# Performance work log

Measured on AMD Instinct MI355X. Metric: run time of the kernel, lower is better.

The kernel has to match this reference:

```python
import jax, jax.numpy as jnp
import numpy as np

SP = 4      # sp_size (number of simulated sequence-parallel ranks)
NH = 16     # num_attention_heads
HD = 64     # head_dim
HS = 1024   # hidden_size
B = 1       # batch
S = 8192    # global sequence length (SP chunks of 2048)


def setup_inputs() -> dict:
    key = jax.random.key(0)
    ks = jax.random.split(key, 9)
    w_scale = 1.0 / np.sqrt(HS)
    def w(k):
        # xavier-ish init, stored as [in, out] so y = x @ W + b
        return jax.random.uniform(k, (HS, HS), jnp.float32, -w_scale, w_scale)
    return {
        'hidden_states': jax.random.normal(ks[0], (B, S, HS), jnp.float32),
        'Wq': w(ks[1]), 'bq': jnp.zeros((HS,), jnp.float32),
        'Wk': w(ks[2]), 'bk': jnp.zeros((HS,), jnp.float32),
        'Wv': w(ks[3]), 'bv': jnp.zeros((HS,), jnp.float32),
        'Wo': w(ks[4]), 'bo': jnp.zeros((HS,), jnp.float32),
    }


def reference(hidden_states, Wq, bq, Wk, bk, Wv, bv, Wo, bo):
    b, s, _ = hidden_states.shape
    sc = s // SP  # per-rank chunk length
    inv_sqrt_hd = 1.0 / np.sqrt(HD)

    def heads(x):
        # [B, S, HS] -> [SP, B, NH, Sc, HD]
        return x.reshape(b, SP, sc, NH, HD).transpose(1, 0, 3, 2, 4)

    q = heads(hidden_states @ Wq + bq)
    k = heads(hidden_states @ Wk + bk)
    v = heads(hidden_states @ Wv + bv)

    out = jnp.zeros_like(q)
    # ring attention: at step i each rank r attends to chunk (r + i) mod SP
    for i in range(SP):
        ki = jnp.roll(k, -i, axis=0)
        vi = jnp.roll(v, -i, axis=0)
        scores = jnp.einsum('sbhqd,sbhkd->sbhqk', q, ki) * inv_sqrt_hd
        probs = jax.nn.softmax(scores, axis=-1)  # per-chunk softmax (faithful to source)
        out = out + jnp.einsum('sbhqk,sbhkd->sbhqd', probs, vi)
    out = out / SP  # source divides accumulated context by sp_size

    # [SP, B, NH, Sc, HD] -> [B, S, NH*HD]
    ctx = out.transpose(1, 0, 3, 2, 4).reshape(b, s, NH * HD)
    return ctx @ Wo + bo
```

## Files before the change

### kernel.cpp

```cpp
#include <hip/hip_runtime.h>

#define DEVINL __device__ __forceinline__

typedef __attribute__((ext_vector_type(8))) short short8;
typedef __attribute__((ext_vector_type(4))) float floatx4;
typedef __attribute__((ext_vector_type(2))) unsigned uintx2;
typedef __attribute__((ext_vector_type(8))) _Float16 halfx8;

DEVINL unsigned short f2bf(float f){
  unsigned u = __builtin_bit_cast(unsigned, f);
  u += 0x7FFFu + ((u >> 16) & 1u);
  return (unsigned short)(u >> 16);
}
DEVINL unsigned pk2(float a, float b){
  unsigned ua = __builtin_bit_cast(unsigned, a);
  unsigned ub = __builtin_bit_cast(unsigned, b);
  ua += 0x7FFFu + ((ua >> 16) & 1u);
  ub += 0x7FFFu + ((ub >> 16) & 1u);
  return (ua >> 16) | (ub & 0xFFFF0000u);
}
DEVINL unsigned pkfast(float a, float b){
  unsigned ua = __builtin_bit_cast(unsigned, a) + 0x8000u;
  unsigned ub = __builtin_bit_cast(unsigned, b) + 0x8000u;
  return __builtin_amdgcn_perm(ub, ua, 0x07060302u);
}
DEVINL unsigned pkh(float a, float b){
  return __builtin_bit_cast(unsigned, __builtin_amdgcn_cvt_pkrtz(a, b));
}
DEVINL float bf2f(unsigned short h){
  unsigned u = ((unsigned)h) << 16;
  return __builtin_bit_cast(float, u);
}
DEVINL void gload_lds16(const void* g, void* l){
  __builtin_amdgcn_global_load_lds((const __attribute__((address_space(1))) void*)g,
                                   (__attribute__((address_space(3))) void*)l, 16, 0, 0);
}
DEVINL int perm2(int k){
  return (((k >> 4) & 1) << 5) | (((k >> 2) & 3) << 3) | (((k >> 5) & 1) << 2) | (k & 3);
}

__global__ void k_detect(const unsigned* __restrict__ w, int* __restrict__ flag){
  __shared__ int cnt;
  if (threadIdx.x == 0) cnt = 0;
  __syncthreads();
  int c = 0;
  for (int i = threadIdx.x; i < 1024; i += 256){
    unsigned e = (w[i] >> 7) & 0xFFu;
    c += (e >= 120u && e <= 132u) ? 1 : 0;
  }
  atomicAdd(&cnt, c);
  __syncthreads();
  if (threadIdx.x == 0) *flag = (cnt > 512) ? 1 : 0;
}

__global__ void k_conv_bf16(const void* __restrict__ src, unsigned short* __restrict__ dst,
                            int n, const int* __restrict__ flag){
  int i = (blockIdx.x * 256 + threadIdx.x) * 8;
  if (i >= n) return;
  if (*flag){
    ((uint4*)dst)[i >> 3] = ((const uint4*)src)[i >> 3];
  } else {
    const float* s = (const float*)src;
    short8 v;
    #pragma unroll
    for (int j = 0; j < 8; j++) v[j] = (short)f2bf(s[i + j]);
    *(short8*)(dst + i) = v;
  }
}

__global__ void k_conv_wT4(const void* __restrict__ s0, const void* __restrict__ s1,
                           const void* __restrict__ s2, const void* __restrict__ s3,
                           unsigned short* __restrict__ d0, unsigned short* __restrict__ d1,
                           unsigned short* __restrict__ d2, unsigned short* __restrict__ d3,
                           const int* __restrict__ flag){
  __shared__ float tile[32][33];
  const void* src; unsigned short* dst;
  switch (blockIdx.z){
    case 0: src = s0; dst = d0; break;
    case 1: src = s1; dst = d1; break;
    case 2: src = s2; dst = d2; break;
    default: src = s3; dst = d3; break;
  }
  const int tx = threadIdx.x & 31, ty = threadIdx.x >> 5;
  const int bx = blockIdx.x, by = blockIdx.y;
  const int isbf = *flag;
  #pragma unroll
  for (int r = 0; r < 32; r += 8){
    int k = by*32 + ty + r, n = bx*32 + tx;
    float v = isbf ? bf2f(((const unsigned short*)src)[k*1024 + n])
                   : ((const float*)src)[k*1024 + n];
    tile[ty + r][tx] = v;
  }
  __syncthreads();
  #pragma unroll
  for (int r = 0; r < 32; r += 8){
    int n = bx*32 + ty + r, k = by*32 + tx;
    dst[n*1024 + k] = f2bf(tile[tx][ty + r]);
  }
}

__global__ void k_conv_b4(const void* __restrict__ s0, const void* __restrict__ s1,
                          const void* __restrict__ s2, const void* __restrict__ s3,
                          float* __restrict__ dst, const int* __restrict__ flag){
  int i = blockIdx.x * 256 + threadIdx.x;
  if (i >= 4096) return;
  int z = i >> 10, j = i & 1023;
  const void* s = (z == 0) ? s0 : (z == 1) ? s1 : (z == 2) ? s2 : s3;
  dst[i] = (*flag) ? bf2f(((const unsigned short*)s)[j]) : ((const float*)s)[j];
}

template<int MODE>
__global__ __launch_bounds__(256, 2) void k_gemm(
    const unsigned short* __restrict__ A, const unsigned short* __restrict__ Bt,
    const float* __restrict__ bias, void* __restrict__ C0, void* __restrict__ C1,
    void* __restrict__ C2, const int* __restrict__ flagp, float scale)
{
  const int K = 1024;
  __shared__ __align__(16) unsigned short As[128*32];
  __shared__ __align__(16) unsigned short Bs[128*32];
  const int tid = threadIdx.x;
  const int lane = tid & 63, wave = tid >> 6;
  const int quad = lane >> 4, l15 = lane & 15;
  const int m0 = blockIdx.x * 128, n0 = blockIdx.y * 128;
  const int wm = (wave >> 1) * 64, wn = (wave & 1) * 64;
  const floatx4 fzero = {0.f, 0.f, 0.f, 0.f};
  floatx4 acc[4][4];
  #pragma unroll
  for (int i = 0; i < 4; i++)
    #pragma unroll
    for (int j = 0; j < 4; j++) acc[i][j] = fzero;

  for (int k0 = 0; k0 < K; k0 += 32){
    __syncthreads();
    #pragma unroll
    for (int rep = 0; rep < 2; rep++){
      int idx = tid + rep*256;
      int row = idx >> 2, c = idx & 3;
      gload_lds16(A  + (size_t)(m0 + row)*K + (k0 + c*8), &As[idx*8]);
      gload_lds16(Bt + (size_t)(n0 + row)*K + (k0 + c*8), &Bs[idx*8]);
    }
    asm volatile("s_waitcnt vmcnt(0)" ::: "memory");
    __syncthreads();
    short8 af[4], bf[4];
    #pragma unroll
    for (int i = 0; i < 4; i++) af[i] = *(const short8*)&As[(wm + i*16 + l15)*32 + quad*8];
    #pragma unroll
    for (int j = 0; j < 4; j++) bf[j] = *(const short8*)&Bs[(wn + j*16 + l15)*32 + quad*8];
    #pragma unroll
    for (int i = 0; i < 4; i++)
      #pragma unroll
      for (int j = 0; j < 4; j++)
        acc[i][j] = __builtin_amdgcn_mfma_f32_16x16x32_bf16(af[i], bf[j], acc[i][j], 0, 0, 0);
  }

  float bs[4];
  #pragma unroll
  for (int j = 0; j < 4; j++) bs[j] = bias[n0 + wn + j*16 + l15];
  const int useBf = (MODE == 1) ? *flagp : 1;
  #pragma unroll
  for (int i = 0; i < 4; i++){
    #pragma unroll
    for (int j = 0; j < 4; j++){
      int n = n0 + wn + j*16 + l15;
      #pragma unroll
      for (int r = 0; r < 4; r++){
        int m = m0 + wm + i*16 + quad*4 + r;
        float v = acc[i][j][r] + bs[j];
        if (MODE == 3){
          int sel = n >> 10, nn = n & 1023;
          if (sel == 0){
            int dd = (nn & 63) ^ ((m & 7) << 3);
            ((unsigned short*)C0)[((size_t)(nn >> 6)*8192 + m)*64 + dd] = f2bf(v * scale);
          } else if (sel == 1){
            int dd = (nn & 63) ^ ((m & 7) << 3);
            ((unsigned short*)C1)[((size_t)(nn >> 6)*8192 + m)*64 + dd] = f2bf(v);
          } else {
            int s2 = perm2(m & 63) ^ ((nn & 7) << 3);
            ((unsigned short*)C2)[(size_t)nn*8192 + (m & ~63) + s2] =
                __builtin_bit_cast(unsigned short, (_Float16)v);
          }
        } else {
          if (useBf) ((unsigned short*)C0)[(size_t)m*1024 + n] = f2bf(v);
          else       ((float*)C0)[(size_t)m*1024 + n] = v;
        }
      }
    }
  }
}

__global__ __launch_bounds__(256, 4) void k_attn2(
    const unsigned short* __restrict__ Qg, const unsigned short* __restrict__ Kg,
    const unsigned short* __restrict__ Vg, _Float16* __restrict__ part)
{
  __shared__ __align__(16) unsigned short KV[2*64*64*2];
  const int tid = threadIdx.x, lane = tid & 63, wave = tid >> 6;
  const int quad = lane >> 4, l15 = lane & 15;
  const int bid = blockIdx.x;
  const int xcd = bid & 7, slot = bid >> 3;
  const int h = xcd*2 + (slot >> 8);
  const int rem = slot & 255;
  const int c = rem >> 6, qt = rem & 63;
  const int sq0 = qt*128;
  const unsigned short* Qp = Qg + (size_t)h*8192*64 + (size_t)sq0*64;
  const char* Kbase = (const char*)(Kg + (size_t)h*8192*64);
  const char* Vbase = (const char*)(Vg + (size_t)h*8192*64);
  const int wq0 = wave * 32;
  const floatx4 fzero = {0.f, 0.f, 0.f, 0.f};

  const int idx0 = tid, idx1 = tid + 256;
  const unsigned voff0 = (unsigned)(idx0 >> 3)*16384u + (unsigned)(idx0 & 7)*16u;
  const unsigned voff1 = (unsigned)(idx1 >> 3)*16384u + (unsigned)(idx1 & 7)*16u;

  auto stage = [&](int buf, int kvs){
    const char* Kt = Kbase + (size_t)kvs*128;
    const char* Vt = Vbase + (size_t)kvs*2;
    char* kd = (char*)KV + buf*8192;
    char* vd = (char*)KV + 16384 + buf*8192;
    gload_lds16(Kt + idx0*16, kd + idx0*16);
    gload_lds16(Kt + idx1*16, kd + idx1*16);
    gload_lds16(Vt + voff0, vd + idx0*16);
    gload_lds16(Vt + voff1, vd + idx1*16);
  };

  short8 qf[2][2];
  #pragma unroll
  for (int mi = 0; mi < 2; mi++)
    #pragma unroll
    for (int ks = 0; ks < 2; ks++){
      int row = wq0 + mi*16 + l15;
      qf[mi][ks] = *(const short8*)&Qp[row*64 + (((ks*4 + quad) ^ (row & 7)))*8];
    }

  stage(0, c*2048);

  const int swz0 = ((    quad) ^ (l15 & 7)) * 16;
  const int swz1 = ((4 + quad) ^ (l15 & 7)) * 16;
  const char* b0 = (const char*)KV + l15*128 + swz0;
  const char* b1 = (const char*)KV + l15*128 + swz1;

  asm volatile("s_waitcnt vmcnt(0)" ::: "memory");
  __syncthreads();

  halfx8 ones;
  {
    union { unsigned short s[8]; halfx8 h; } u;
    #pragma unroll
    for (int j = 0; j < 8; j++) u.s[j] = 0x3C00;
    ones = u.h;
  }

  floatx4 Oc[2][4], Ol[2];
  #pragma unroll
  for (int mi = 0; mi < 2; mi++){
    Ol[mi] = fzero;
    #pragma unroll
    for (int di = 0; di < 4; di++) Oc[mi][di] = fzero;
  }

#define ATTN_TILE(CUR, KT)                                                            \
  {                                                                                   \
    asm volatile("s_waitcnt vmcnt(0)" ::: "memory");              \
    __syncthreads();                                           \
    if ((KT) < 31)                                                                    \
      stage((CUR) ^ 1, c*2048 + ((KT) + 1)*64);          \
    halfx8 pf[2][2];                                                                  \
    {                                                                                 \
      floatx4 S0[4], S1[4];                                                           \
      _Pragma("unroll")                                                               \
      for (int ni = 0; ni < 4; ni++){ S0[ni] = fzero; S1[ni] = fzero; }               \
      _Pragma("unroll")                                                               \
      for (int ni = 0; ni < 4; ni++){                                                 \
        short8 kf0 = *(const short8*)(b0 + (CUR)*8192 + ni*2048);                     \
        short8 kf1 = *(const short8*)(b1 + (CUR)*8192 + ni*2048);                     \
        S0[ni] = __builtin_amdgcn_mfma_f32_16x16x32_bf16(kf0, qf[0][0], S0[ni], 0, 0, 0); \
        S0[ni] = __builtin_amdgcn_mfma_f32_16x16x32_bf16(kf1, qf[0][1], S0[ni], 0, 0, 0); \
        S1[ni] = __builtin_amdgcn_mfma_f32_16x16x32_bf16(kf0, qf[1][0], S1[ni], 0, 0, 0); \
        S1[ni] = __builtin_amdgcn_mfma_f32_16x16x32_bf16(kf1, qf[1][1], S1[ni], 0, 0, 0); \
      }                                                                               \
      _Pragma("unroll")                                                               \
      for (int ni = 0; ni < 4; ni++)                                                  \
        _Pragma("unroll")                                                             \
        for (int r = 0; r < 4; r++){                                                  \
          S0[ni][r] = __builtin_amdgcn_exp2f(S0[ni][r]);                              \
          S1[ni][r] = __builtin_amdgcn_exp2f(S1[ni][r]);                              \
        }                                                                             \
      _Pragma("unroll")                                                               \
      for (int ks = 0; ks < 2; ks++){                                                 \
        union { unsigned u[4]; halfx8 h; } cv;                                        \
        cv.u[0] = pkh(S0[ks  ][0], S0[ks  ][1]);                                      \
        cv.u[1] = pkh(S0[ks  ][2], S0[ks  ][3]);                                      \
        cv.u[2] = pkh(S0[2+ks][0], S0[2+ks][1]);                                      \
        cv.u[3] = pkh(S0[2+ks][2], S0[2+ks][3]);                                      \
        pf[0][ks] = cv.h;                                                             \
        cv.u[0] = pkh(S1[ks  ][0], S1[ks  ][1]);                                      \
        cv.u[1] = pkh(S1[ks  ][2], S1[ks  ][3]);                                      \
        cv.u[2] = pkh(S1[2+ks][0], S1[2+ks][1]);                                      \
        cv.u[3] = pkh(S1[2+ks][2], S1[2+ks][3]);                                      \
        pf[1][ks] = cv.h;                                                             \
      }                                                                               \
    }                                                                                 \
    _Pragma("unroll")                                                                 \
    for (int ks = 0; ks < 2; ks++){                                                   \
      const char* vb = ks ? b1 : b0;                                                  \
      _Pragma("unroll")                                                               \
      for (int di = 0; di < 4; di++){                                                 \
        halfx8 vf = __builtin_bit_cast(halfx8,                                        \
            *(const short8*)(vb + (16384 + (CUR)*8192) + di*2048));                   \
        Oc[0][di] = __builtin_amdgcn_mfma_f32_16x16x32_f16(vf, pf[0][ks], Oc[0][di], 0, 0, 0); \
        Oc[1][di] = __builtin_amdgcn_mfma_f32_16x16x32_f16(vf, pf[1][ks], Oc[1][di], 0, 0, 0); \
      }                                                                               \
      Ol[0] = __builtin_amdgcn_mfma_f32_16x16x32_f16(ones, pf[0][ks], Ol[0], 0, 0, 0); \
      Ol[1] = __builtin_amdgcn_mfma_f32_16x16x32_f16(ones, pf[1][ks], Ol[1], 0, 0, 0); \
    }                                                                                 \
  }

  for (int kt = 0; kt < 32; kt += 2){
    ATTN_TILE(0, kt)
    ATTN_TILE(1, kt + 1)
  }
#undef ATTN_TILE

  #pragma unroll
  for (int mi = 0; mi < 2; mi++){
    float inv = __builtin_amdgcn_rcpf(Ol[mi][0]);
    int q = sq0 + wq0 + mi*16 + l15;
    _Float16* dst = part + ((size_t)c*8192 + q)*1024 + h*64;
    #pragma unroll
    for (int di = 0; di < 4; di++){
      union { _Float16 hh[4]; uintx2 u; } w;
      #pragma unroll
      for (int r = 0; r < 4; r++) w.hh[r] = (_Float16)(Oc[mi][di][r] * inv);
      *(uintx2*)(dst + di*16 + quad*4) = w.u;
    }
  }
}

__global__ void k_reduce(const _Float16* __restrict__ part, unsigned short* __restrict__ ctx){
  const size_t N = (size_t)8192*1024;
  size_t i = ((size_t)blockIdx.x*256 + threadIdx.x)*8;
  if (i >= N) return;
  halfx8 a = *(const halfx8*)(part + i);
  halfx8 b = *(const halfx8*)(part + N + i);
  halfx8 c = *(const halfx8*)(part + 2*N + i);
  halfx8 d = *(const halfx8*)(part + 3*N + i);
  short8 o;
  #pragma unroll
  for (int j = 0; j < 8; j++){
    float s = ((float)a[j] + (float)b[j]) + ((float)c[j] + (float)d[j]);
    o[j] = (short)f2bf(s * 0.25f);
  }
  *(short8*)&ctx[i] = o;
}

__global__ __launch_bounds__(256, 2) void k_attn(
    const unsigned short* __restrict__ Qg, const unsigned short* __restrict__ Kg,
    const unsigned short* __restrict__ Vg, unsigned short* __restrict__ ctx)
{
  __shared__ __align__(16) unsigned short Qs[256*64];
  __shared__ __align__(16) unsigned short Ks[2][64*64];
  __shared__ __align__(16) unsigned short Vs[2][64*64];
  const int tid = threadIdx.x, lane = tid & 63, wave = tid >> 6;
  const int quad = lane >> 4, l15 = lane & 15;
  const int bid = blockIdx.x;
  const int xcd = bid & 7, slot = bid >> 3;
  const int h = xcd*2 + (slot >> 5);
  const int rem = slot & 31, rchunk = rem >> 3, qt = rem & 7;
  const int sq0 = rchunk*2048 + qt*256;
  const char* Qbase = (const char*)(Qg + (size_t)h*8192*64 + (size_t)sq0*64);
  const char* Kbase = (const char*)(Kg + (size_t)h*8192*64);
  const char* Vbase = (const char*)(Vg + (size_t)h*8192*64);
  const int wq0 = wave * 64;
  const floatx4 fzero = {0.f, 0.f, 0.f, 0.f};

  const int idx0 = tid, idx1 = tid + 256;
  const size_t voff0 = (size_t)(idx0 >> 3)*16384 + (idx0 & 7)*16;
  const size_t voff1 = (size_t)(idx1 >> 3)*16384 + (idx1 & 7)*16;

  auto stage = [&](int buf, int kvs){
    const char* Kt = Kbase + (size_t)kvs*128;
    const char* Vt = Vbase + (size_t)kvs*2;
    char* kd = (char*)Ks[buf];
    char* vd = (char*)Vs[buf];
    gload_lds16(Kt + idx0*16, kd + idx0*16);
    gload_lds16(Kt + idx1*16, kd + idx1*16);
    gload_lds16(Vt + voff0, vd + idx0*16);
    gload_lds16(Vt + voff1, vd + idx1*16);
  };

  #pragma unroll
  for (int rep = 0; rep < 8; rep++){
    int idx = tid + rep*256;
    gload_lds16(Qbase + idx*16, (char*)Qs + idx*16);
  }
  stage(0, rchunk*2048);
  asm volatile("s_waitcnt vmcnt(0)" ::: "memory");
  __syncthreads();

  short8 qf[4][2];
  #pragma unroll
  for (int mi = 0; mi < 4; mi++)
    #pragma unroll
    for (int ks = 0; ks < 2; ks++){
      int row = wq0 + mi*16 + l15;
      qf[mi][ks] = *(const short8*)&Qs[row*64 + (((ks*4 + quad) ^ (row & 7)))*8];
    }

  halfx8 ones;
  {
    union { unsigned short s[8]; halfx8 h; } u;
    #pragma unroll
    for (int j = 0; j < 8; j++) u.s[j] = 0x3C00;
    ones = u.h;
  }

  floatx4 Of[4][4];
  #pragma unroll
  for (int mi = 0; mi < 4; mi++)
    #pragma unroll
    for (int di = 0; di < 4; di++) Of[mi][di] = fzero;

  for (int i = 0; i < 4; i++){
    floatx4 Oc[4][4], Ol[4];
    #pragma unroll
    for (int mi = 0; mi < 4; mi++){
      Ol[mi] = fzero;
      #pragma unroll
      for (int di = 0; di < 4; di++) Oc[mi][di] = fzero;
    }

    for (int kt = 0; kt < 32; kt++){
      const int t = i*32 + kt, cur = t & 1;
      asm volatile("s_waitcnt vmcnt(0)" ::: "memory");
      __syncthreads();
      if (t < 127){
        int t1 = t + 1;
        int kvs = ((rchunk + (t1 >> 5)) & 3)*2048 + (t1 & 31)*64;
        stage(cur ^ 1, kvs);
      }

      halfx8 pf[4][2];
      #pragma unroll
      for (int mi = 0; mi < 4; mi++){
        floatx4 St[4];
        #pragma unroll
        for (int ni = 0; ni < 4; ni++) St[ni] = fzero;
        #pragma unroll
        for (int ks = 0; ks < 2; ks++)
          #pragma unroll
          for (int ni = 0; ni < 4; ni++){
            int krow = ni*16 + l15;
            short8 kf = *(const short8*)&Ks[cur][krow*64 + (((ks*4 + quad) ^ (krow & 7)))*8];
            St[ni] = __builtin_amdgcn_mfma_f32_16x16x32_bf16(kf, qf[mi][ks], St[ni], 0, 0, 0);
          }
        #pragma unroll
        for (int ni = 0; ni < 4; ni++)
          #pragma unroll
          for (int r = 0; r < 4; r++)
            St[ni][r] = __builtin_amdgcn_exp2f(St[ni][r]);
        #pragma unroll
        for (int ks = 0; ks < 2; ks++){
          union { unsigned u[4]; halfx8 h; } cv;
          cv.u[0] = pkh(St[ks  ][0], St[ks  ][1]);
          cv.u[1] = pkh(St[ks  ][2], St[ks  ][3]);
          cv.u[2] = pkh(St[2+ks][0], St[2+ks][1]);
          cv.u[3] = pkh(St[2+ks][2], St[2+ks][3]);
          pf[mi][ks] = cv.h;
        }
      }

      #pragma unroll
      for (int ks = 0; ks < 2; ks++){
        #pragma unroll
        for (int di = 0; di < 4; di++){
          int vrow = di*16 + l15;
          halfx8 vf = __builtin_bit_cast(halfx8,
              *(const short8*)&Vs[cur][vrow*64 + (((ks*4 + quad) ^ (vrow & 7)))*8]);
          #pragma unroll
          for (int mi = 0; mi < 4; mi++)
            Oc[mi][di] = __builtin_amdgcn_mfma_f32_16x16x32_f16(vf, pf[mi][ks], Oc[mi][di], 0, 0, 0);
        }
        #pragma unroll
        for (int mi = 0; mi < 4; mi++)
          Ol[mi] = __builtin_amdgcn_mfma_f32_16x16x32_f16(ones, pf[mi][ks], Ol[mi], 0, 0, 0);
      }
    }

    #pragma unroll
    for (int mi = 0; mi < 4; mi++){
      float inv = __builtin_amdgcn_rcpf(Ol[mi][0]);
      #pragma unroll
      for (int di = 0; di < 4; di++)
        #pragma unroll
        for (int r = 0; r < 4; r++) Of[mi][di][r] += Oc[mi][di][r] * inv;
    }
  }

  #pragma unroll
  for (int mi = 0; mi < 4; mi++){
    int q = sq0 + wq0 + mi*16 + l15;
    #pragma unroll
    for (int di = 0; di < 4; di++){
      uintx2 w;
      w[0] = pk2(Of[mi][di][0]*0.25f, Of[mi][di][1]*0.25f);
      w[1] = pk2(Of[mi][di][2]*0.25f, Of[mi][di][3]*0.25f);
      *(uintx2*)&ctx[(size_t)q*1024 + h*64 + di*16 + quad*4] = w;
    }
  }
}

extern "C" void kernel_launch(void* const* d_in, const int* in_sizes, int n_in,
                              void* d_out, int out_size, void* d_ws, size_t ws_size,
                              hipStream_t stream)
{
  (void)in_sizes; (void)n_in; (void)out_size;
  char* ws = (char*)d_ws;
  size_t off = 0;
  auto alloc = [&](size_t bytes) -> char* {
    char* p = ws + off;
    off = (off + bytes + 255) & ~(size_t)255;
    return p;
  };
  int* flag            = (int*)alloc(4);
  unsigned short* hsb  = (unsigned short*)alloc((size_t)8192*1024*2);
  unsigned short* wqt  = (unsigned short*)alloc((size_t)1024*1024*2);
  unsigned short* wkt  = (unsigned short*)alloc((size_t)1024*1024*2);
  unsigned short* wvt  = (unsigned short*)alloc((size_t)1024*1024*2);
  unsigned short* wot  = (unsigned short*)alloc((size_t)1024*1024*2);
  float* biasAll       = (float*)alloc(4096*4);
  unsigned short* Qb   = (unsigned short*)alloc((size_t)16*8192*64*2);
  unsigned short* Kb   = (unsigned short*)alloc((size_t)16*8192*64*2);
  unsigned short* Vb   = (unsigned short*)alloc((size_t)16*8192*64*2);
  unsigned short* ctxb = (unsigned short*)alloc((size_t)8192*1024*2);
  _Float16* part       = (_Float16*)alloc((size_t)4*8192*1024*2);
  const bool wide = (off <= ws_size);

  k_detect<<<1, 256, 0, stream>>>((const unsigned*)d_in[0], flag);
  k_conv_bf16<<<4096, 256, 0, stream>>>(d_in[0], hsb, 8192*1024, flag);
  k_conv_wT4<<<dim3(32,32,4), 256, 0, stream>>>(d_in[1], d_in[3], d_in[5], d_in[7],
                                                wqt, wkt, wvt, wot, flag);
  k_conv_b4<<<16, 256, 0, stream>>>(d_in[2], d_in[4], d_in[6], d_in[8], biasAll, flag);

  const float Cs = 0.18033688011112042f;
  k_gemm<3><<<dim3(64, 24), 256, 0, stream>>>(hsb, wqt, biasAll, Qb, Kb, Vb, nullptr, Cs);

  if (wide){
    k_attn2<<<4096, 256, 0, stream>>>(Qb, Kb, Vb, part);
    k_reduce<<<4096, 256, 0, stream>>>(part, ctxb);
  } else {
    k_attn<<<512, 256, 0, stream>>>(Qb, Kb, Vb, ctxb);
  }

  k_gemm<1><<<dim3(64, 8), 256, 0, stream>>>(ctxb, wot, biasAll + 3072, d_out,
                                             nullptr, nullptr, flag, 1.0f);
}
```

Measured before the change: 500.3 us.

## Fuse partial-context reduction into output projection GEMM and add MFMA priority hints

Removes the separate reduce kernel: a new GEMM mode sums the four fp16 partial attention outputs, scales, converts to bf16 while staging the A tile into shared memory. This avoids writing and rereading the intermediate ctx buffer and one launch, but each N-tile block now rereads all four partials through synchronous loads instead of async LDS loads. The attention tile also raises wave priority around MFMA sections via s_setprio.

```diff
diff --git a/kernel.cpp b/kernel.cpp
--- a/kernel.cpp
+++ b/kernel.cpp
@@ -132,12 +132,40 @@
 
   for (int k0 = 0; k0 < K; k0 += 32){
     __syncthreads();
-    #pragma unroll
-    for (int rep = 0; rep < 2; rep++){
-      int idx = tid + rep*256;
-      int row = idx >> 2, c = idx & 3;
-      gload_lds16(A  + (size_t)(m0 + row)*K + (k0 + c*8), &As[idx*8]);
-      gload_lds16(Bt + (size_t)(n0 + row)*K + (k0 + c*8), &Bs[idx*8]);
+    if constexpr (MODE == 2){
+      #pragma unroll
+      for (int rep = 0; rep < 2; rep++){
+        int idx = tid + rep*256;
+        int row = idx >> 2, c = idx & 3;
+        gload_lds16(Bt + (size_t)(n0 + row)*K + (k0 + c*8), &Bs[idx*8]);
+      }
+      const _Float16* P = (const _Float16*)A;
+      const size_t N1 = (size_t)8192*1024;
+      #pragma unroll
+      for (int rep = 0; rep < 2; rep++){
+        int idx = tid + rep*256;
+        int row = idx >> 2, c = idx & 3;
+        const _Float16* p = P + (size_t)(m0 + row)*K + (k0 + c*8);
+        halfx8 a0 = *(const halfx8*)(p);
+        halfx8 a1 = *(const halfx8*)(p + N1);
+        halfx8 a2 = *(const halfx8*)(p + 2*N1);
+        halfx8 a3 = *(const halfx8*)(p + 3*N1);
+        short8 o;
+        #pragma unroll
+        for (int j = 0; j < 8; j++){
+          float s = (((float)a0[j] + (float)a1[j]) + ((float)a2[j] + (float)a3[j])) * 0.25f;
+          o[j] = (short)f2bf(s);
+        }
+        *(short8*)&As[idx*8] = o;
+      }
+    } else {
+      #pragma unroll
+      for (int rep = 0; rep < 2; rep++){
+        int idx = tid + rep*256;
+        int row = idx >> 2, c = idx & 3;
+        gload_lds16(A  + (size_t)(m0 + row)*K + (k0 + c*8), &As[idx*8]);
+        gload_lds16(Bt + (size_t)(n0 + row)*K + (k0 + c*8), &Bs[idx*8]);
+      }
     }
     asm volatile("s_waitcnt vmcnt(0)" ::: "memory");
     __syncthreads();
@@ -156,7 +184,7 @@
   float bs[4];
   #pragma unroll
   for (int j = 0; j < 4; j++) bs[j] = bias[n0 + wn + j*16 + l15];
-  const int useBf = (MODE == 1) ? *flagp : 1;
+  const int useBf = (MODE == 3) ? 1 : *flagp;
   #pragma unroll
   for (int i = 0; i < 4; i++){
     #pragma unroll
@@ -268,6 +296,7 @@
       floatx4 S0[4], S1[4];                                                           \
       _Pragma("unroll")                                                               \
       for (int ni = 0; ni < 4; ni++){ S0[ni] = fzero; S1[ni] = fzero; }               \
+      __builtin_amdgcn_s_setprio(1);                                                  \
       _Pragma("unroll")                                                               \
       for (int ni = 0; ni < 4; ni++){                                                 \
         short8 kf0 = *(const short8*)(b0 + (CUR)*8192 + ni*2048);                     \
@@ -277,6 +306,7 @@
         S1[ni] = __builtin_amdgcn_mfma_f32_16x16x32_bf16(kf0, qf[1][0], S1[ni], 0, 0, 0); \
         S1[ni] = __builtin_amdgcn_mfma_f32_16x16x32_bf16(kf1, qf[1][1], S1[ni], 0, 0, 0); \
       }                                                                               \
+      __builtin_amdgcn_s_setprio(0);                                                  \
       _Pragma("unroll")                                                               \
       for (int ni = 0; ni < 4; ni++)                                                  \
         _Pragma("unroll")                                                             \
@@ -299,6 +329,7 @@
         pf[1][ks] = cv.h;                                                             \
       }                                                                               \
     }                                                                                 \
+    __builtin_amdgcn_s_setprio(1);                                                    \
     _Pragma("unroll")                                                                 \
     for (int ks = 0; ks < 2; ks++){                                                   \
       const char* vb = ks ? b1 : b0;                                                  \
@@ -312,6 +343,7 @@
       Ol[0] = __builtin_amdgcn_mfma_f32_16x16x32_f16(ones, pf[0][ks], Ol[0], 0, 0, 0); \
       Ol[1] = __builtin_amdgcn_mfma_f32_16x16x32_f16(ones, pf[1][ks], Ol[1], 0, 0, 0); \
     }                                                                                 \
+    __builtin_amdgcn_s_setprio(0);                                                    \
   }
 
   for (int kt = 0; kt < 32; kt += 2){
@@ -333,23 +365,6 @@
       *(uintx2*)(dst + di*16 + quad*4) = w.u;
     }
   }
-}
-
-__global__ void k_reduce(const _Float16* __restrict__ part, unsigned short* __restrict__ ctx){
-  const size_t N = (size_t)8192*1024;
-  size_t i = ((size_t)blockIdx.x*256 + threadIdx.x)*8;
-  if (i >= N) return;
-  halfx8 a = *(const halfx8*)(part + i);
-  halfx8 b = *(const halfx8*)(part + N + i);
-  halfx8 c = *(const halfx8*)(part + 2*N + i);
-  halfx8 d = *(const halfx8*)(part + 3*N + i);
-  short8 o;
-  #pragma unroll
-  for (int j = 0; j < 8; j++){
-    float s = ((float)a[j] + (float)b[j]) + ((float)c[j] + (float)d[j]);
-    o[j] = (short)f2bf(s * 0.25f);
-  }
-  *(short8*)&ctx[i] = o;
 }
 
 __global__ __launch_bounds__(256, 2) void k_attn(
@@ -545,11 +560,12 @@
 
   if (wide){
     k_attn2<<<4096, 256, 0, stream>>>(Qb, Kb, Vb, part);
-    k_reduce<<<4096, 256, 0, stream>>>(part, ctxb);
+    k_gemm<2><<<dim3(64, 8), 256, 0, stream>>>((const unsigned short*)part, wot,
+                                               biasAll + 3072, d_out,
+                                               nullptr, nullptr, flag, 1.0f);
   } else {
     k_attn<<<512, 256, 0, stream>>>(Qb, Kb, Vb, ctxb);
-  }
-
-  k_gemm<1><<<dim3(64, 8), 256, 0, stream>>>(ctxb, wot, biasAll + 3072, d_out,
-                                             nullptr, nullptr, flag, 1.0f);
-}
+    k_gemm<1><<<dim3(64, 8), 256, 0, stream>>>(ctxb, wot, biasAll + 3072, d_out,
+                                               nullptr, nullptr, flag, 1.0f);
+  }
+}
```

Measured after the change: 485.9 us. 1.03x faster.
